# Optimization experiments

Measured on AMD Instinct MI355X. Metric: run time of the kernel, lower is better.

Reference implementation:

```python
import jax, jax.numpy as jnp
import numpy as np

N_NODES = 50000
N_EDGES = 800000
IN_F = 256
HID = 64          # hidden_features; GAT layers output 2*HID = 128
OUT_F = 2
NUM_GRAPHS = 32
NEG_SLOPE = 0.2   # PyG GATConv default


def setup_inputs() -> dict:
    key = jax.random.key(0)
    ks = jax.random.split(key, 16)
    g = 2 * HID
    def glorot(k, shape):
        fan_in = shape[0] if len(shape) > 1 else shape[0]
        return jax.random.normal(k, shape, dtype=jnp.float32) / np.sqrt(fan_in)
    return {
        "x": jax.random.normal(ks[0], (N_NODES, IN_F), dtype=jnp.float32),
        "edge_index": jax.random.randint(ks[1], (2, N_EDGES), 0, N_NODES, dtype=jnp.int64),
        "batch": jnp.sort(jax.random.randint(ks[2], (N_NODES,), 0, NUM_GRAPHS, dtype=jnp.int64)),
        "W1": glorot(ks[3], (IN_F, g)),
        "as1": glorot(ks[4], (g,)),
        "ad1": glorot(ks[5], (g,)),
        "b1": jnp.zeros((g,), jnp.float32),
        "W2": glorot(ks[6], (g, g)),
        "as2": glorot(ks[7], (g,)),
        "ad2": glorot(ks[8], (g,)),
        "b2": jnp.zeros((g,), jnp.float32),
        "lw1": glorot(ks[9], (g, HID)),
        "lb1": jnp.zeros((HID,), jnp.float32),
        "lw2": glorot(ks[10], (HID, OUT_F)),
        "lb2": jnp.zeros((OUT_F,), jnp.float32),
    }


def _gat_conv(x, W, a_src, a_dst, bias, src, dst, n):
    # Single-head PyG GATConv: linear -> per-edge LeakyReLU attention logits ->
    # softmax over incoming edges per destination -> weighted scatter-sum.
    h = x @ W                                   # [N, F]
    es = h @ a_src                              # [N] source attention terms
    ed = h @ a_dst                              # [N] destination attention terms
    e = jax.nn.leaky_relu(es[src] + ed[dst], NEG_SLOPE)   # [E]
    m = jax.ops.segment_max(e, dst, num_segments=n)
    m = jnp.where(jnp.isfinite(m), m, 0.0)      # guard empty segments
    ex = jnp.exp(e - m[dst])
    den = jax.ops.segment_sum(ex, dst, num_segments=n)
    alpha = ex / (den[dst] + 1e-16)             # PyG softmax epsilon
    out = jax.ops.segment_sum(alpha[:, None] * h[src], dst, num_segments=n)
    return out + bias


def reference(x, edge_index, batch, W1, as1, ad1, b1, W2, as2, ad2, b2, lw1, lb1, lw2, lb2):
    n = x.shape[0]
    loops = jnp.arange(n, dtype=edge_index.dtype)
    src = jnp.concatenate([edge_index[0], loops])   # add_self_loops=True (PyG default)
    dst = jnp.concatenate([edge_index[1], loops])

    h = jax.nn.selu(_gat_conv(x, W1, as1, ad1, b1, src, dst, n))
    h = jax.nn.selu(_gat_conv(h, W2, as2, ad2, b2, src, dst, n))

    # global_mean_pool over graph-batch vector
    sums = jax.ops.segment_sum(h, batch, num_segments=NUM_GRAPHS)
    cnts = jax.ops.segment_sum(jnp.ones((n,), h.dtype), batch, num_segments=NUM_GRAPHS)
    pooled = sums / jnp.maximum(cnts, 1.0)[:, None]     # [B, 2*HID]

    z = jax.nn.selu(pooled)
    z = jax.nn.selu(z @ lw1 + lb1)
    z = z @ lw2 + lb2
    return jax.nn.log_softmax(z, axis=-1)
```

## Files before the change

### kernel.cpp

```cpp
#include <hip/hip_runtime.h>
#include <hip/hip_bf16.h>
#include <math.h>

#define N_NODES 50000
#define N_EDGES 800000
#define IN_F 256
#define G 128
#define NHID 64
#define NGRAPH 32
#define NBUCK ((N_NODES + 255) / 256)
#define CAPB 8192
#define CELL 64
#define EPB 4096
#define NBA ((N_EDGES + EPB - 1) / EPB)
#define RQ 8
#define RQSH 13

typedef __hip_bfloat16 bf16;
typedef unsigned short ushort;
typedef __attribute__((ext_vector_type(8))) short short8;
typedef __attribute__((ext_vector_type(4))) float f32x4;

__device__ __forceinline__ float bf2f(ushort u) {
    union { unsigned u; float f; } c; c.u = ((unsigned)u) << 16; return c.f;
}
__device__ __forceinline__ ushort f2bf(float f) {
    unsigned u = __float_as_uint(f);
    u += 0x7FFFu + ((u >> 16) & 1u);
    return (ushort)(u >> 16);
}
__device__ __forceinline__ float ldf(const void* p, long i, int f32) {
    return f32 ? ((const float*)p)[i] : bf2f(((const ushort*)p)[i]);
}
__device__ __forceinline__ int ldi(const void* p, long i, int i64) {
    return i64 ? (int)((const long long*)p)[i] : ((const int*)p)[i];
}

__device__ __forceinline__ float selu_f(float x) {
    const float sc = 1.0507009873554805f, al = 1.6732632423543772f;
    return x > 0.f ? sc * x : sc * al * expm1f(x);
}

typedef const __attribute__((address_space(1))) void gas_void;
typedef __attribute__((address_space(3))) void las_void;
__device__ __forceinline__ void stage16(const void* g, void* l) {
    __builtin_amdgcn_global_load_lds((gas_void*)g, (las_void*)l, 16, 0, 0);
}

__device__ __forceinline__ void edge_sd(const void* __restrict__ ei, int e, int i64,
                                        int& s, int& d) {
    s = ldi(ei, e, i64);
    d = ldi(ei, (long)N_EDGES + e, i64);
    s = min(max(s, 0), N_NODES - 1);
    d = min(max(d, 0), N_NODES - 1);
}


__global__ __launch_bounds__(256) void binA_kernel(
    const void* __restrict__ ei, unsigned* __restrict__ pairs,
    int* __restrict__ cnts, int* __restrict__ flags,
    const void* __restrict__ x,
    const void* __restrict__ W1, const void* __restrict__ W2,
    ushort* __restrict__ wt1, ushort* __restrict__ wt2) {
    __shared__ int cnt[256], lofs[256], pcur[256];
    __shared__ unsigned stage[EPB];
    __shared__ int s_i64, s_f32;
    int t = threadIdx.x;

    if (t < 64) {
        const unsigned* wu = (const unsigned*)ei;
        long j = 1 + (long)t * 24986;
        unsigned long long bal = __ballot(wu[j] != 0u);
        if (t == 0) s_i64 = (__popcll(bal) < 16) ? 1 : 0;
    } else if (t < 128) {
        const unsigned* xu = (const unsigned*)x;
        unsigned u = xu[(long)(t - 64) * 100000];
        unsigned e = (u >> 23) & 0xFF;
        unsigned long long bal = __ballot(u == 0u || (e >= 100 && e <= 140));
        if (t == 64) s_f32 = (__popcll(bal) >= 32) ? 1 : 0;
    }
    cnt[t] = 0;
    __syncthreads();
    int i64 = s_i64, f32 = s_f32;
    if (blockIdx.x == 0 && t == 0) { flags[0] = f32; flags[1] = i64; }

    int e0 = blockIdx.x * EPB;
    int nE = min(EPB, N_EDGES - e0);
    int sj[EPB / 256], dj[EPB / 256];
#pragma unroll
    for (int j = 0; j < EPB / 256; j++) {
        int idx = j * 256 + t;
        if (idx < nE) {
            edge_sd(ei, e0 + idx, i64, sj[j], dj[j]);
            atomicAdd(&cnt[dj[j] >> 8], 1);
        } else dj[j] = -1;
    }
    __syncthreads();
    lofs[t] = cnt[t];
    for (int off = 1; off < 256; off <<= 1) {
        __syncthreads();
        int v = (t >= off) ? lofs[t - off] : 0;
        __syncthreads();
        lofs[t] += v;
    }
    __syncthreads();
    int excl = lofs[t] - cnt[t];
    __syncthreads();
    lofs[t] = excl;
    pcur[t] = excl;
    __syncthreads();
#pragma unroll
    for (int j = 0; j < EPB / 256; j++) {
        if (dj[j] >= 0) {
            int b = dj[j] >> 8;
            int lp = atomicAdd(&pcur[b], 1);
            stage[lp] = (unsigned)sj[j] | ((unsigned)(dj[j] & 255) << 16) |
                        ((unsigned)b << 24);
        }
    }
    __syncthreads();
    for (int i = t; i < nE; i += 256) {
        unsigned p = stage[i];
        int b = p >> 24;
        int off2 = i - lofs[b];
        if (off2 < CELL)
            pairs[((size_t)b * NBA + blockIdx.x) * CELL + off2] = p;
    }
    if (t < NBUCK) cnts[(size_t)t * NBA + blockIdx.x] = min(cnt[t], CELL);

    int wi = blockIdx.x * 256 + t;
    if (wi < IN_F * G + G * G) {
        const void* W; ushort* wtp; int idx;
        if (wi < IN_F * G) { W = W1; wtp = wt1; idx = wi; }
        else { W = W2; wtp = wt2; idx = wi - IN_F * G; }
        int k = idx >> 7, n = idx & (G - 1);
        float wv = ldf(W, idx, f32);
        ushort h = f2bf(wv);
        ushort lo = f2bf(wv - bf2f(h));
        int c = k >> 5, q = (k >> 3) & 3, j = k & 7;
        int nt = n >> 4, n16 = n & 15;
        int lane = q * 16 + n16;
        size_t base = ((size_t)c * 16 + nt * 2) * 512 + lane * 8 + j;
        wtp[base] = h;
        wtp[base + 512] = lo;
    }
}

__device__ __forceinline__ void binB_body(
    const unsigned* __restrict__ pairs, const int* __restrict__ cnts,
    int2* __restrict__ rowse, ushort* __restrict__ srcs,
    int b, int t, int* cntq , int* sscan , int* ccnt ) {
    if (t < NBA) ccnt[t] = cnts[(size_t)b * NBA + t];
#pragma unroll
    for (int j = 0; j < RQ; j++) cntq[t * RQ + j] = 0;
    int node = b * 256 + t;
    int valid = (node < N_NODES) ? 1 : 0;
    __syncthreads();
    if (valid) atomicAdd(&cntq[t * RQ + (node >> RQSH)], 1);
    if (t < NBA) {
        const unsigned* cp = pairs + ((size_t)b * NBA + t) * CELL;
        int n = ccnt[t];
        for (int i = 0; i < n; i++) {
            unsigned r = cp[i];
            int d = (r >> 16) & 255, q = (int)(r & 0xFFFFu) >> RQSH;
            atomicAdd(&cntq[d * RQ + q], 1);
        }
    }
    __syncthreads();
    int c[RQ], lex[RQ], st = 0;
#pragma unroll
    for (int j = 0; j < RQ; j++) { c[j] = cntq[t * RQ + j]; lex[j] = st; st += c[j]; }
    sscan[t] = st;
    for (int off = 1; off < 256; off <<= 1) {
        __syncthreads();
        int v = (t >= off) ? sscan[t - off] : 0;
        __syncthreads();
        sscan[t] += v;
    }
    __syncthreads();
    int excl = sscan[t] - st;
    int base = b * CAPB;
    if (valid) rowse[node] = make_int2(base + excl, base + excl + st);
#pragma unroll
    for (int j = 0; j < RQ; j++) cntq[t * RQ + j] = base + excl + lex[j];
    __syncthreads();
    if (valid) {
        int pos = atomicAdd(&cntq[t * RQ + (node >> RQSH)], 1);
        srcs[pos] = (ushort)node;
    }
    if (t < NBA) {
        const unsigned* cp = pairs + ((size_t)b * NBA + t) * CELL;
        int n = ccnt[t];
        for (int i = 0; i < n; i++) {
            unsigned r = cp[i];
            int d = (r >> 16) & 255, q = (int)(r & 0xFFFFu) >> RQSH;
            int pos = atomicAdd(&cntq[d * RQ + q], 1);
            srcs[pos] = (ushort)(r & 0xFFFFu);
        }
    }
}

template <int K, bool AF32>
__device__ __forceinline__ void gemm_body(
    int bid, const void* __restrict__ A, const ushort* __restrict__ wt,
    unsigned* __restrict__ H2, const int* __restrict__ flags,
    const void* __restrict__ aS, const void* __restrict__ aD,
    float2* __restrict__ es2, short8* sB8) {
    constexpr int NC = K / 32;
    int wave = threadIdx.x >> 6, lane = threadIdx.x & 63;
    int quad = lane >> 4, n16 = lane & 15;
    int rb = bid * 64 + wave * 16;
    int rowa = min(rb + n16, N_NODES - 1);
    f32x4 acc[8];
#pragma unroll
    for (int t = 0; t < 8; t++) acc[t] = (f32x4){0.f, 0.f, 0.f, 0.f};

    for (int c = 0; c < NC; c++) {
#pragma unroll
        for (int i = 0; i < 4; i++) {
            int fw = wave * 4 + i;
            stage16(wt + ((size_t)c * 16 + fw) * 512 + lane * 8, &sB8[fw * 64]);
        }
        float av[8];
        if (AF32) {
            const float* ap = (const float*)A + (size_t)rowa * K + c * 32 + quad * 8;
            f32x4 a0 = *(const f32x4*)ap;
            f32x4 a1 = *(const f32x4*)(ap + 4);
#pragma unroll
            for (int j = 0; j < 4; j++) { av[j] = a0[j]; av[j + 4] = a1[j]; }
        } else {
            const ushort* ap = (const ushort*)A + (size_t)rowa * K + c * 32 + quad * 8;
#pragma unroll
            for (int j = 0; j < 8; j++) av[j] = bf2f(ap[j]);
        }
        short8 ahi, alo;
#pragma unroll
        for (int j = 0; j < 8; j++) {
            ushort h = f2bf(av[j]);
            ahi[j] = (short)h;
            alo[j] = (short)f2bf(av[j] - bf2f(h));
        }
        __syncthreads();
#pragma unroll
        for (int nt = 0; nt < 8; nt++) {
            short8 bh = sB8[(nt * 2 + 0) * 64 + lane];
            short8 bl = sB8[(nt * 2 + 1) * 64 + lane];
            acc[nt] = __builtin_amdgcn_mfma_f32_16x16x32_bf16(ahi, bh, acc[nt], 0, 0, 0);
            acc[nt] = __builtin_amdgcn_mfma_f32_16x16x32_bf16(ahi, bl, acc[nt], 0, 0, 0);
            acc[nt] = __builtin_amdgcn_mfma_f32_16x16x32_bf16(alo, bh, acc[nt], 0, 0, 0);
        }
        __syncthreads();
    }

    int f32 = flags[0];
    float asv[8], adv[8];
#pragma unroll
    for (int nt = 0; nt < 8; nt++) {
        asv[nt] = ldf(aS, nt * 16 + n16, f32);
        adv[nt] = ldf(aD, nt * 16 + n16, f32);
    }
#pragma unroll
    for (int r = 0; r < 4; r++) {
        int ro = rb + quad * 4 + r;
        float s = 0.f, dv = 0.f;
#pragma unroll
        for (int nt = 0; nt < 8; nt++) {
            s += acc[nt][r] * asv[nt];
            dv += acc[nt][r] * adv[nt];
        }
        if (ro < N_NODES) {
#pragma unroll
            for (int nt = 0; nt < 4; nt++) {
                unsigned pack = (unsigned)f2bf(acc[nt][r]) |
                                ((unsigned)f2bf(acc[nt + 4][r]) << 16);
                H2[(size_t)ro * 64 + nt * 16 + n16] = pack;
            }
        }
#pragma unroll
        for (int off = 8; off; off >>= 1) {
            s += __shfl_xor(s, off);
            dv += __shfl_xor(dv, off);
        }
        if (n16 == 0 && ro < N_NODES) es2[ro] = make_float2(s, dv);
    }
}

template <int K>
__global__ __launch_bounds__(256, 3) void binB_gemm_kernel(
    const unsigned* __restrict__ pairs, const int* __restrict__ cnts,
    int2* __restrict__ rowse, ushort* __restrict__ srcs,
    const void* __restrict__ A, const ushort* __restrict__ wt,
    unsigned* __restrict__ H2, const int* __restrict__ flags,
    const void* __restrict__ aS, const void* __restrict__ aD,
    float2* __restrict__ es2) {
    __shared__ short8 sB8[16 * 64];
    __shared__ int s_cntq[256 * RQ];
    __shared__ int s_scan[256], s_ccnt[NBA];
    if (blockIdx.x < NBUCK) {
        binB_body(pairs, cnts, rowse, srcs, blockIdx.x, threadIdx.x,
                  s_cntq, s_scan, s_ccnt);
        return;
    }
    int bid = blockIdx.x - NBUCK;
    if (flags[0]) gemm_body<K, true>(bid, A, wt, H2, flags, aS, aD, es2, sB8);
    else          gemm_body<K, false>(bid, A, wt, H2, flags, aS, aD, es2, sB8);
}

template <int K>
__global__ __launch_bounds__(256, 3) void gemm_mfma_kernel(
    const void* __restrict__ A, const ushort* __restrict__ wt,
    unsigned* __restrict__ H2, int a_mode, const int* __restrict__ flags,
    const void* __restrict__ aS, const void* __restrict__ aD,
    float2* __restrict__ es2, float* __restrict__ zbuf) {
    __shared__ short8 sB8[16 * 64];
    if (zbuf != nullptr && blockIdx.x == 0) {
        for (int i = threadIdx.x; i < NGRAPH * G; i += 256) zbuf[i] = 0.f;
    }
    int af32 = (a_mode == 2) ? 0 : flags[0];
    if (af32) gemm_body<K, true>(blockIdx.x, A, wt, H2, flags, aS, aD, es2, sB8);
    else      gemm_body<K, false>(blockIdx.x, A, wt, H2, flags, aS, aD, es2, sB8);
}

template <int POOL>
__global__ __launch_bounds__(256) void gat_agg_kernel(
    const unsigned* __restrict__ h2, const int2* __restrict__ rowse,
    const ushort* __restrict__ srcs, const float2* __restrict__ es2,
    const void* __restrict__ bias, ushort* __restrict__ outb,
    const void* __restrict__ batch, float* __restrict__ gsum,
    const int* __restrict__ flags) {
    int node = blockIdx.x * 4 + (threadIdx.x >> 6);
    if (node >= N_NODES) return;
    int l = threadIdx.x & 63;
    int2 se = rowse[node];
    int start = se.x, end = se.y;
    float edd = es2[node].y;
    float m = -INFINITY, den = 0.f;
    float acc0 = 0.f, acc1 = 0.f;
    for (int c0 = start; c0 < end; c0 += 64) {
        int cn = min(end - c0, 64);
        int s = 0; float v = -INFINITY;
        if (l < cn) {
            s = (int)srcs[c0 + l];
            v = es2[s].x + edd;
            v = v >= 0.f ? v : 0.2f * v;
        }
        float mc = v;
#pragma unroll
        for (int off = 32; off; off >>= 1) mc = fmaxf(mc, __shfl_xor(mc, off));
        float mnew = fmaxf(m, mc);
        float scale = expf(m - mnew);
        float p = (l < cn) ? expf(v - mnew) : 0.f;
        float lsum = p;
#pragma unroll
        for (int off = 32; off; off >>= 1) lsum += __shfl_xor(lsum, off);
        den = den * scale + lsum;
        acc0 *= scale; acc1 *= scale;
        int cnr = (cn + 7) & ~7;
        for (int i = 0; i < cnr; i += 8) {
            int sis[8]; float pis[8]; unsigned hv[8];
#pragma unroll
            for (int j = 0; j < 8; j++) {
                sis[j] = __builtin_amdgcn_readlane(s, i + j);
                pis[j] = __uint_as_float(
                    __builtin_amdgcn_readlane(__float_as_uint(p), i + j));
            }
#pragma unroll
            for (int j = 0; j < 8; j++)
                hv[j] = h2[(size_t)sis[j] * 64 + l];
#pragma unroll
            for (int j = 0; j < 8; j++) {
                acc0 += pis[j] * bf2f((ushort)(hv[j] & 0xFFFFu));
                acc1 += pis[j] * bf2f((ushort)(hv[j] >> 16));
            }
        }
        m = mnew;
    }
    float inv = 1.f / (den + 1e-16f);
    int f32 = flags[0];
    float o0 = selu_f(acc0 * inv + ldf(bias, l, f32));
    float o1 = selu_f(acc1 * inv + ldf(bias, l + 64, f32));
    if (POOL) {
        int gid = min(max(ldi(batch, node, flags[1]), 0), NGRAPH - 1);
        atomicAdd(&gsum[gid * G + l], o0);
        atomicAdd(&gsum[gid * G + 64 + l], o1);
    } else {
        outb[(size_t)node * G + l]      = f2bf(o0);
        outb[(size_t)node * G + l + 64] = f2bf(o1);
    }
}

__global__ void head_kernel(const float* __restrict__ gsum, const void* __restrict__ batch,
                            const void* __restrict__ lw1, const void* __restrict__ lb1,
                            const void* __restrict__ lw2, const void* __restrict__ lb2,
                            float* __restrict__ out, const int* __restrict__ flags) {
    int g = blockIdx.x, t = threadIdx.x;
    int f32 = flags[0], i64 = flags[1];
    __shared__ float z[G];
    __shared__ float z1[NHID];
    __shared__ float z2[2];
    __shared__ int sb[2];
    if (t < 2) {
        int target = g + t;
        int lo = 0, hi = N_NODES;
        while (lo < hi) {
            int mid = (lo + hi) >> 1;
            int v = ldi(batch, mid, i64);
            if (v < target) lo = mid + 1; else hi = mid;
        }
        sb[t] = lo;
    }
    __syncthreads();
    float cnt = fmaxf((float)(sb[1] - sb[0]), 1.0f);
    z[t]      = selu_f(gsum[g * G + t] / cnt);
    z[t + 64] = selu_f(gsum[g * G + 64 + t] / cnt);
    __syncthreads();
    float a = ldf(lb1, t, f32);
    for (int k = 0; k < G; k++) a += z[k] * ldf(lw1, k * NHID + t, f32);
    z1[t] = selu_f(a);
    __syncthreads();
    if (t < 2) {
        float s = ldf(lb2, t, f32);
        for (int j = 0; j < NHID; j++) s += z1[j] * ldf(lw2, j * 2 + t, f32);
        z2[t] = s;
    }
    __syncthreads();
    if (t == 0) {
        float mx = fmaxf(z2[0], z2[1]);
        float l = mx + logf(expf(z2[0] - mx) + expf(z2[1] - mx));
        out[g * 2 + 0] = z2[0] - l;
        out[g * 2 + 1] = z2[1] - l;
    }
}

extern "C" void kernel_launch(void* const* d_in, const int* in_sizes, int n_in,
                              void* d_out, int out_size, void* d_ws, size_t ws_size,
                              hipStream_t stream) {
    const void* x    = d_in[0];
    const void* ei   = d_in[1];
    const void* batch= d_in[2];
    const void* W1   = d_in[3];
    const void* as1  = d_in[4];
    const void* ad1  = d_in[5];
    const void* b1   = d_in[6];
    const void* W2   = d_in[7];
    const void* as2  = d_in[8];
    const void* ad2  = d_in[9];
    const void* b2   = d_in[10];
    const void* lw1  = d_in[11];
    const void* lb1  = d_in[12];
    const void* lw2  = d_in[13];
    const void* lb2  = d_in[14];
    float* out = (float*)d_out;

    char* w = (char*)d_ws;
    size_t off = 0;
    auto alloc = [&](size_t bytes) -> char* {
        char* p = w + off;
        off = (off + bytes + 255) & ~(size_t)255;
        return p;
    };
    int*      flags  = (int*)alloc(256);
    unsigned* h2     = (unsigned*)alloc((size_t)N_NODES * 64 * 4);
    ushort*   abuf   = (ushort*)alloc((size_t)N_NODES * G * 2);
    float2*   es2    = (float2*)alloc((size_t)N_NODES * 8);
    int2*     rowse  = (int2*)alloc((size_t)N_NODES * 8);
    unsigned* pairs  = (unsigned*)alloc((size_t)NBUCK * NBA * CELL * 4);
    int*      cnts   = (int*)alloc((size_t)NBUCK * NBA * 4);
    ushort*   srcs   = (ushort*)alloc((size_t)NBUCK * CAPB * 2);
    float*    gsum   = (float*)alloc((size_t)NGRAPH * G * 4);
    ushort*   wt1    = (ushort*)alloc((size_t)IN_F * G * 2 * 2);
    ushort*   wt2    = (ushort*)alloc((size_t)G * G * 2 * 2);

    unsigned gemm_grid = (N_NODES + 63) / 64;
    unsigned agg_grid = (N_NODES + 3) / 4;

    binA_kernel<<<NBA, 256, 0, stream>>>(ei, pairs, cnts, flags, x, W1, W2, wt1, wt2);
    binB_gemm_kernel<IN_F><<<NBUCK + gemm_grid, 256, 0, stream>>>(
        pairs, cnts, rowse, srcs, x, wt1, h2, flags, as1, ad1, es2);
    gat_agg_kernel<0><<<agg_grid, 256, 0, stream>>>(h2, rowse, srcs, es2, b1, abuf,
                                                    nullptr, nullptr, flags);
    gemm_mfma_kernel<G><<<gemm_grid, 256, 0, stream>>>(abuf, wt2, h2, 2, flags,
                                                       as2, ad2, es2, gsum);
    gat_agg_kernel<1><<<agg_grid, 256, 0, stream>>>(h2, rowse, srcs, es2, b2, nullptr,
                                                    batch, gsum, flags);
    head_kernel<<<NGRAPH, 64, 0, stream>>>(gsum, batch, lw1, lb1, lw2, lb2, out, flags);
}
```

Before: 338.1 us.

## Store GAT hidden features as custom 8-bit floats and split gather across half-waves

The projected node features are now stored as a custom FP8-like format (4 exponent bits, 3 mantissa bits, rounded) instead of bf16. This halves the bytes per source row that the aggregation kernel gathers. Each half-wave now handles alternate edges, reading a 128-byte row with 32 lanes, decoding four values per word, and combining the halves with a cross-lane shuffle at the end. The decode folds a fixed exponent bias into the attention weight. The cost is lower precision in the aggregated features, which risks accuracy tolerance, plus extra encode and decode ALU work.

```diff
diff --git a/kernel.cpp b/kernel.cpp
--- a/kernel.cpp
+++ b/kernel.cpp
@@ -39,6 +39,21 @@
 __device__ __forceinline__ float selu_f(float x) {
     const float sc = 1.0507009873554805f, al = 1.6732632423543772f;
     return x > 0.f ? sc * x : sc * al * expm1f(x);
+}
+
+__device__ __forceinline__ unsigned enc8(float f) {
+    unsigned u = __float_as_uint(f);
+    unsigned s = (u >> 24) & 0x80u;
+    unsigned a = u & 0x7FFFFFFFu;
+    unsigned v = a + 0x7FFFFu + ((a >> 20) & 1u);
+    int e8 = (int)(v >> 23) - 120;
+    unsigned mb;
+    if (e8 >= 1) {
+        mb = (e8 > 15) ? 0x7Eu : (((unsigned)e8 << 3) | ((v >> 20) & 7u));
+    } else {
+        mb = (unsigned)(int)(__uint_as_float(a) * 512.0f + 0.5f);
+    }
+    return s | mb;
 }
 
 typedef const __attribute__((address_space(1))) void gas_void;
@@ -203,7 +218,7 @@
 template <int K, bool AF32>
 __device__ __forceinline__ void gemm_body(
     int bid, const void* __restrict__ A, const ushort* __restrict__ wt,
-    unsigned* __restrict__ H2, const int* __restrict__ flags,
+    unsigned* __restrict__ H8, const int* __restrict__ flags,
     const void* __restrict__ aS, const void* __restrict__ aD,
     float2* __restrict__ es2, short8* sB8) {
     constexpr int NC = K / 32;
@@ -269,12 +284,12 @@
             dv += acc[nt][r] * adv[nt];
         }
         if (ro < N_NODES) {
-#pragma unroll
-            for (int nt = 0; nt < 4; nt++) {
-                unsigned pack = (unsigned)f2bf(acc[nt][r]) |
-                                ((unsigned)f2bf(acc[nt + 4][r]) << 16);
-                H2[(size_t)ro * 64 + nt * 16 + n16] = pack;
-            }
+            unsigned w0 = enc8(acc[0][r]) | (enc8(acc[2][r]) << 8) |
+                          (enc8(acc[4][r]) << 16) | (enc8(acc[6][r]) << 24);
+            unsigned w1 = enc8(acc[1][r]) | (enc8(acc[3][r]) << 8) |
+                          (enc8(acc[5][r]) << 16) | (enc8(acc[7][r]) << 24);
+            H8[(size_t)ro * 32 + n16] = w0;
+            H8[(size_t)ro * 32 + 16 + n16] = w1;
         }
 #pragma unroll
         for (int off = 8; off; off >>= 1) {
@@ -290,7 +305,7 @@
     const unsigned* __restrict__ pairs, const int* __restrict__ cnts,
     int2* __restrict__ rowse, ushort* __restrict__ srcs,
     const void* __restrict__ A, const ushort* __restrict__ wt,
-    unsigned* __restrict__ H2, const int* __restrict__ flags,
+    unsigned* __restrict__ H8, const int* __restrict__ flags,
     const void* __restrict__ aS, const void* __restrict__ aD,
     float2* __restrict__ es2) {
     __shared__ short8 sB8[16 * 64];
@@ -302,14 +317,14 @@
         return;
     }
     int bid = blockIdx.x - NBUCK;
-    if (flags[0]) gemm_body<K, true>(bid, A, wt, H2, flags, aS, aD, es2, sB8);
-    else          gemm_body<K, false>(bid, A, wt, H2, flags, aS, aD, es2, sB8);
+    if (flags[0]) gemm_body<K, true>(bid, A, wt, H8, flags, aS, aD, es2, sB8);
+    else          gemm_body<K, false>(bid, A, wt, H8, flags, aS, aD, es2, sB8);
 }
 
 template <int K>
 __global__ __launch_bounds__(256, 3) void gemm_mfma_kernel(
     const void* __restrict__ A, const ushort* __restrict__ wt,
-    unsigned* __restrict__ H2, int a_mode, const int* __restrict__ flags,
+    unsigned* __restrict__ H8, int a_mode, const int* __restrict__ flags,
     const void* __restrict__ aS, const void* __restrict__ aD,
     float2* __restrict__ es2, float* __restrict__ zbuf) {
     __shared__ short8 sB8[16 * 64];
@@ -317,13 +332,13 @@
         for (int i = threadIdx.x; i < NGRAPH * G; i += 256) zbuf[i] = 0.f;
     }
     int af32 = (a_mode == 2) ? 0 : flags[0];
-    if (af32) gemm_body<K, true>(blockIdx.x, A, wt, H2, flags, aS, aD, es2, sB8);
-    else      gemm_body<K, false>(blockIdx.x, A, wt, H2, flags, aS, aD, es2, sB8);
+    if (af32) gemm_body<K, true>(blockIdx.x, A, wt, H8, flags, aS, aD, es2, sB8);
+    else      gemm_body<K, false>(blockIdx.x, A, wt, H8, flags, aS, aD, es2, sB8);
 }
 
 template <int POOL>
 __global__ __launch_bounds__(256) void gat_agg_kernel(
-    const unsigned* __restrict__ h2, const int2* __restrict__ rowse,
+    const unsigned* __restrict__ h8, const int2* __restrict__ rowse,
     const ushort* __restrict__ srcs, const float2* __restrict__ es2,
     const void* __restrict__ bias, ushort* __restrict__ outb,
     const void* __restrict__ batch, float* __restrict__ gsum,
@@ -331,11 +346,13 @@
     int node = blockIdx.x * 4 + (threadIdx.x >> 6);
     if (node >= N_NODES) return;
     int l = threadIdx.x & 63;
+    int w = l & 31;
+    int half = l >> 5;
     int2 se = rowse[node];
     int start = se.x, end = se.y;
     float edd = es2[node].y;
     float m = -INFINITY, den = 0.f;
-    float acc0 = 0.f, acc1 = 0.f;
+    float acc[4] = {0.f, 0.f, 0.f, 0.f};
     for (int c0 = start; c0 < end; c0 += 64) {
         int cn = min(end - c0, 64);
         int s = 0; float v = -INFINITY;
@@ -354,38 +371,55 @@
 #pragma unroll
         for (int off = 32; off; off >>= 1) lsum += __shfl_xor(lsum, off);
         den = den * scale + lsum;
-        acc0 *= scale; acc1 *= scale;
-        int cnr = (cn + 7) & ~7;
-        for (int i = 0; i < cnr; i += 8) {
-            int sis[8]; float pis[8]; unsigned hv[8];
+#pragma unroll
+        for (int k = 0; k < 4; k++) acc[k] *= scale;
+        int cnr = (cn + 15) & ~15;
+        for (int i = 0; i < cnr; i += 16) {
+            int sis[16]; unsigned pbit[16]; unsigned hv[8];
+#pragma unroll
+            for (int j = 0; j < 16; j++) {
+                sis[j] = __builtin_amdgcn_readlane(s, i + j);
+                unsigned pb = __builtin_amdgcn_readlane(__float_as_uint(p), i + j);
+                pbit[j] = (pb >= 0x00800000u) ? pb + (120u << 23) : 0u;
+            }
 #pragma unroll
             for (int j = 0; j < 8; j++) {
-                sis[j] = __builtin_amdgcn_readlane(s, i + j);
-                pis[j] = __uint_as_float(
-                    __builtin_amdgcn_readlane(__float_as_uint(p), i + j));
+                int row = half ? sis[2 * j + 1] : sis[2 * j];
+                hv[j] = h8[(size_t)row * 32 + w];
             }
 #pragma unroll
-            for (int j = 0; j < 8; j++)
-                hv[j] = h2[(size_t)sis[j] * 64 + l];
-#pragma unroll
             for (int j = 0; j < 8; j++) {
-                acc0 += pis[j] * bf2f((ushort)(hv[j] & 0xFFFFu));
-                acc1 += pis[j] * bf2f((ushort)(hv[j] >> 16));
+                float pv = __uint_as_float(half ? pbit[2 * j + 1] : pbit[2 * j]);
+                unsigned wd = hv[j];
+#pragma unroll
+                for (int k = 0; k < 4; k++) {
+                    unsigned b = (wd >> (8 * k)) & 0xFFu;
+                    unsigned fb = ((b & 0x7Fu) << 20) | ((b & 0x80u) << 24);
+                    acc[k] += pv * __uint_as_float(fb);
+                }
             }
         }
         m = mnew;
     }
     float inv = 1.f / (den + 1e-16f);
+#pragma unroll
+    for (int k = 0; k < 4; k++) acc[k] += __shfl_xor(acc[k], 32);
     int f32 = flags[0];
-    float o0 = selu_f(acc0 * inv + ldf(bias, l, f32));
-    float o1 = selu_f(acc1 * inv + ldf(bias, l + 64, f32));
-    if (POOL) {
-        int gid = min(max(ldi(batch, node, flags[1]), 0), NGRAPH - 1);
-        atomicAdd(&gsum[gid * G + l], o0);
-        atomicAdd(&gsum[gid * G + 64 + l], o1);
-    } else {
-        outb[(size_t)node * G + l]      = f2bf(o0);
-        outb[(size_t)node * G + l + 64] = f2bf(o1);
+    if (l < 32) {
+        if (POOL) {
+            int gid = min(max(ldi(batch, node, flags[1]), 0), NGRAPH - 1);
+#pragma unroll
+            for (int k = 0; k < 4; k++) {
+                int c = w + 32 * k;
+                atomicAdd(&gsum[gid * G + c], selu_f(acc[k] * inv + ldf(bias, c, f32)));
+            }
+        } else {
+#pragma unroll
+            for (int k = 0; k < 4; k++) {
+                int c = w + 32 * k;
+                outb[(size_t)node * G + c] = f2bf(selu_f(acc[k] * inv + ldf(bias, c, f32)));
+            }
+        }
     }
 }
 
@@ -460,7 +494,7 @@
         return p;
     };
     int*      flags  = (int*)alloc(256);
-    unsigned* h2     = (unsigned*)alloc((size_t)N_NODES * 64 * 4);
+    unsigned* h8     = (unsigned*)alloc((size_t)N_NODES * 32 * 4);
     ushort*   abuf   = (ushort*)alloc((size_t)N_NODES * G * 2);
     float2*   es2    = (float2*)alloc((size_t)N_NODES * 8);
     int2*     rowse  = (int2*)alloc((size_t)N_NODES * 8);
@@ -476,12 +510,12 @@
 
     binA_kernel<<<NBA, 256, 0, stream>>>(ei, pairs, cnts, flags, x, W1, W2, wt1, wt2);
     binB_gemm_kernel<IN_F><<<NBUCK + gemm_grid, 256, 0, stream>>>(
-        pairs, cnts, rowse, srcs, x, wt1, h2, flags, as1, ad1, es2);
-    gat_agg_kernel<0><<<agg_grid, 256, 0, stream>>>(h2, rowse, srcs, es2, b1, abuf,
+        pairs, cnts, rowse, srcs, x, wt1, h8, flags, as1, ad1, es2);
+    gat_agg_kernel<0><<<agg_grid, 256, 0, stream>>>(h8, rowse, srcs, es2, b1, abuf,
                                                     nullptr, nullptr, flags);
-    gemm_mfma_kernel<G><<<gemm_grid, 256, 0, stream>>>(abuf, wt2, h2, 2, flags,
+    gemm_mfma_kernel<G><<<gemm_grid, 256, 0, stream>>>(abuf, wt2, h8, 2, flags,
                                                        as2, ad2, es2, gsum);
-    gat_agg_kernel<1><<<agg_grid, 256, 0, stream>>>(h2, rowse, srcs, es2, b2, nullptr,
+    gat_agg_kernel<1><<<agg_grid, 256, 0, stream>>>(h8, rowse, srcs, es2, b2, nullptr,
                                                     batch, gsum, flags);
     head_kernel<<<NGRAPH, 64, 0, stream>>>(gsum, batch, lw1, lb1, lw2, lb2, out, flags);
 }
```

New measurement: 413.8 us. +22.4%, slower.
